# Optimization experiments

Hardware: AMD Instinct MI355X
Metric: run time of the kernel (lower is better)

Reference implementation:

```python
import jax, jax.numpy as jnp
import numpy as np

H = 1024      # hidden_size
E = 8         # num_experts
I = 1024      # moe_intermediate_size
SI = 2816     # shared_expert_intermediate_size
B, S = 2, 2048


def setup_inputs() -> dict:
    key = jax.random.key(0)
    ks = jax.random.split(key, 10)
    sc = lambda fan_in: 1.0 / np.sqrt(fan_in)
    return {
        "hidden_states": jax.random.normal(ks[0], (B, S, H), dtype=jnp.float32),
        "gate_w": jax.random.normal(ks[1], (E, H), dtype=jnp.float32) * sc(H),
        "wg": jax.random.normal(ks[2], (E, I, H), dtype=jnp.float32) * sc(H),   # gate_proj per expert
        "wu": jax.random.normal(ks[3], (E, I, H), dtype=jnp.float32) * sc(H),   # up_proj per expert
        "wd": jax.random.normal(ks[4], (E, H, I), dtype=jnp.float32) * sc(I),   # down_proj per expert
        "swg": jax.random.normal(ks[5], (SI, H), dtype=jnp.float32) * sc(H),    # shared gate_proj
        "swu": jax.random.normal(ks[6], (SI, H), dtype=jnp.float32) * sc(H),    # shared up_proj
        "swd": jax.random.normal(ks[7], (H, SI), dtype=jnp.float32) * sc(SI),   # shared down_proj
        "shared_gate_w": jax.random.normal(ks[8], (1, H), dtype=jnp.float32) * sc(H),
        "top_k": 2,
    }


def reference(hidden_states, gate_w, wg, wu, wd, swg, swu, swd, shared_gate_w, top_k):
    b, s, h = hidden_states.shape
    flat = hidden_states.reshape(-1, h)                      # [T,H]
    # router
    logits = flat @ gate_w.T                                 # [T,E]
    probs = jax.nn.softmax(logits, axis=-1)
    vals, idx = jax.lax.top_k(probs, top_k)                  # [T,K]
    vals = vals / jnp.sum(vals, axis=-1, keepdims=True)      # norm_topk_prob
    # combine weights scattered to full expert dim: [T,E]
    combine = jnp.sum(jax.nn.one_hot(idx, E, dtype=flat.dtype) * vals[..., None], axis=1)
    # dense per-expert SwiGLU FFN over all tokens, masked-combined (same math)
    g = jax.nn.silu(jnp.einsum("th,eih->eti", flat, wg))     # [E,T,I]
    u = jnp.einsum("th,eih->eti", flat, wu)
    eo = jnp.einsum("eti,ehi->eth", g * u, wd)               # [E,T,H]
    expert_out = jnp.einsum("te,eth->th", combine, eo)       # [T,H]
    # shared expert with sigmoid gate
    shared = (jax.nn.silu(flat @ swg.T) * (flat @ swu.T)) @ swd.T   # [T,H]
    sgate = jax.nn.sigmoid(flat @ shared_gate_w.T)           # [T,1]
    out = expert_out + sgate * shared
    return out.reshape(b, s, h)
```

## Files before the change

kernel.cpp:

```cpp
#include <hip/hip_runtime.h>
#include <stdint.h>

#define TT  4096
#define HD  1024
#define NE  8
#define ID  1024
#define SID 2816

typedef short s16x8 __attribute__((ext_vector_type(8)));
typedef float f32x4 __attribute__((ext_vector_type(4)));
typedef float f32x4v __attribute__((ext_vector_type(4)));
typedef unsigned short u16x4 __attribute__((ext_vector_type(4)));

__device__ __forceinline__ ushort f2bf(float f) {
  uint32_t u = __float_as_uint(f);
  u += 0x7FFFu + ((u >> 16) & 1u);
  return (ushort)(u >> 16);
}

__device__ __forceinline__ float bf2f(ushort u) {
  return __uint_as_float((uint32_t)u << 16);
}

__device__ __forceinline__ void gll16(const ushort* g, ushort* l) {
  __builtin_amdgcn_global_load_lds(
      (const __attribute__((address_space(1))) void*)g,
      (__attribute__((address_space(3))) void*)l, 16, 0, 0);
}

struct CvtArgs {
  const float* src[7];
  ushort* dst[7];
  int n[7];
};

__global__ __launch_bounds__(256) void cvt_all(CvtArgs a) {
  int t = blockIdx.y;
  int i = (blockIdx.x * 256 + threadIdx.x) * 4;
  if (i >= a.n[t]) return;
  f32x4v v = *(const f32x4v*)(a.src[t] + i);
  u16x4 o;
  o.x = f2bf(v.x); o.y = f2bf(v.y); o.z = f2bf(v.z); o.w = f2bf(v.w);
  *(u16x4*)(a.dst[t] + i) = o;
}

__global__ __launch_bounds__(256) void router_k(
    const float* __restrict__ X, const float* __restrict__ gw,
    const float* __restrict__ sgw,
    int* __restrict__ topki, float* __restrict__ topkw,
    float* __restrict__ sgate) {
  __shared__ float gwL[(NE + 1) * HD];
  #pragma unroll
  for (int i = 0; i < NE * HD / 1024; i++) {
    int idx = i * 1024 + threadIdx.x * 4;
    *(f32x4*)&gwL[idx] = *(const f32x4*)&gw[idx];
  }
  {
    int idx = threadIdx.x * 4;
    if (idx < HD) *(f32x4*)&gwL[NE * HD + idx] = *(const f32x4*)&sgw[idx];
  }
  __syncthreads();

  const int wave = threadIdx.x >> 6, lane = threadIdx.x & 63;
  #pragma unroll
  for (int tt = 0; tt < 4; tt++) {
    const int t = blockIdx.x * 16 + wave * 4 + tt;
    const float* x = X + (size_t)t * HD;
    float acc[NE + 1];
    #pragma unroll
    for (int e = 0; e <= NE; e++) acc[e] = 0.f;
    #pragma unroll
    for (int p = 0; p < HD / 256; p++) {
      const int k = p * 256 + lane * 4;
      f32x4 xv = *(const f32x4*)&x[k];
      #pragma unroll
      for (int e = 0; e < NE; e++) {
        f32x4 g = *(const f32x4*)&gwL[e * HD + k];
        acc[e] += xv.x * g.x + xv.y * g.y + xv.z * g.z + xv.w * g.w;
      }
      f32x4 s = *(const f32x4*)&gwL[NE * HD + k];
      acc[NE] += xv.x * s.x + xv.y * s.y + xv.z * s.z + xv.w * s.w;
    }
    #pragma unroll
    for (int off = 32; off > 0; off >>= 1)
      #pragma unroll
      for (int e = 0; e <= NE; e++)
        acc[e] += __shfl_xor(acc[e], off, 64);
    if (lane == 0) {
      float m = acc[0];
      #pragma unroll
      for (int e = 1; e < NE; e++) m = fmaxf(m, acc[e]);
      float p[NE];
      #pragma unroll
      for (int e = 0; e < NE; e++) p[e] = __expf(acc[e] - m);
      int i1 = 0;
      #pragma unroll
      for (int e = 1; e < NE; e++) if (p[e] > p[i1]) i1 = e;
      int i2 = (i1 == 0) ? 1 : 0;
      #pragma unroll
      for (int e = 0; e < NE; e++) if (e != i1 && p[e] > p[i2]) i2 = e;
      float inv = 1.f / (p[i1] + p[i2]);
      topki[2 * t] = i1; topki[2 * t + 1] = i2;
      topkw[2 * t] = p[i1] * inv; topkw[2 * t + 1] = p[i2] * inv;
      sgate[t] = 1.f / (1.f + __expf(-acc[NE]));
    }
  }
}

__global__ __launch_bounds__(1024) void binning_k(
    const int* __restrict__ topki, const float* __restrict__ topkw,
    int* __restrict__ cnt, int* __restrict__ offs,
    int* __restrict__ tokmap, float* __restrict__ wmap,
    int* __restrict__ smap) {
  __shared__ int h[NE];
  __shared__ int base[NE];
  const int tid = threadIdx.x;
  if (tid < NE) h[tid] = 0;
  __syncthreads();
  int my_e[8];
  #pragma unroll
  for (int i = 0; i < 8; i++) {
    int s = i * 1024 + tid;
    my_e[i] = topki[s];
    atomicAdd(&h[my_e[i]], 1);
  }
  __syncthreads();
  if (tid == 0) {
    int o = 0;
    for (int e = 0; e < NE; e++) {
      base[e] = o; offs[e] = o; cnt[e] = h[e]; o += h[e];
    }
  }
  __syncthreads();
  #pragma unroll
  for (int i = 0; i < 8; i++) {
    int s = i * 1024 + tid;
    int pos = atomicAdd(&base[my_e[i]], 1);
    tokmap[pos] = s >> 1;
    wmap[pos] = topkw[s];
    smap[s] = pos;
  }
}

constexpr int BM = 128, BN = 128, BK = 32;

template <bool GATHER>
__device__ __forceinline__ void gu_core(
    const ushort* __restrict__ A, const ushort* __restrict__ Wg,
    const ushort* __restrict__ Wu, ushort* __restrict__ Hout,
    const int* __restrict__ tokmap, int cnt, int seg,
    int mb, int nb, int N, int K) {
  const int m0 = mb * BM;
  if (m0 >= cnt) return;
  const int n0 = nb * BN;

  __shared__ ushort lA[3][BM * BK];
  __shared__ ushort lBg[3][BN * BK];
  __shared__ ushort lBu[3][BN * BK];

  const int tid = threadIdx.x;
  const int wave = tid >> 6, lane = tid & 63;
  const int wm = (wave >> 1) * 64, wn = (wave & 1) * 64;

  const int ar0 = wave * 32 + (lane >> 2);
  const int ar1 = ar0 + 16;
  const int kc = ((lane & 3) ^ ((lane >> 3) & 3)) * 8;

  const ushort *a0p, *a1p;
  if (GATHER) {
    int m_ = m0 + ar0;
    int tk0 = (m_ < cnt) ? tokmap[seg + m_] : 0;
    m_ = m0 + ar1;
    int tk1 = (m_ < cnt) ? tokmap[seg + m_] : 0;
    a0p = A + (size_t)tk0 * K + kc;
    a1p = A + (size_t)tk1 * K + kc;
  } else {
    a0p = A + (size_t)(m0 + ar0) * K + kc;
    a1p = A + (size_t)(m0 + ar1) * K + kc;
  }
  const ushort* bg0 = Wg + (size_t)(n0 + ar0) * K + kc;
  const ushort* bg1 = Wg + (size_t)(n0 + ar1) * K + kc;
  const ushort* bu0 = Wu + (size_t)(n0 + ar0) * K + kc;
  const ushort* bu1 = Wu + (size_t)(n0 + ar1) * K + kc;

  f32x4 accG[4][4], accU[4][4];
  #pragma unroll
  for (int i = 0; i < 4; i++)
    #pragma unroll
    for (int j = 0; j < 4; j++) {
      accG[i][j] = f32x4{0.f, 0.f, 0.f, 0.f};
      accU[i][j] = f32x4{0.f, 0.f, 0.f, 0.f};
    }

  const int lr = lane & 15;
  const int lk = (((lane >> 4) ^ ((lr >> 1) & 3))) * 8;
  const int w32 = wave * 32;

  auto stage = [&](int b, int k0) {
    gll16(a0p + k0, &lA[b][w32 * BK]);
    gll16(a1p + k0, &lA[b][(w32 + 16) * BK]);
    gll16(bg0 + k0, &lBg[b][w32 * BK]);
    gll16(bg1 + k0, &lBg[b][(w32 + 16) * BK]);
    gll16(bu0 + k0, &lBu[b][w32 * BK]);
    gll16(bu1 + k0, &lBu[b][(w32 + 16) * BK]);
  };

  const int nt = K / BK;
  stage(0, 0);
  stage(1, BK);
  int buf = 0;
  for (int t = 0; t < nt; t++) {
    if (t + 2 < nt) {
      int nb2 = buf + 2; if (nb2 >= 3) nb2 -= 3;
      stage(nb2, (t + 2) * BK);
      asm volatile("s_waitcnt vmcnt(12)" ::: "memory");
    } else if (t + 1 < nt) {
      asm volatile("s_waitcnt vmcnt(6)" ::: "memory");
    } else {
      asm volatile("s_waitcnt vmcnt(0)" ::: "memory");
    }
    __builtin_amdgcn_s_barrier();

    s16x8 af[4], bgf[4], buf_[4];
    #pragma unroll
    for (int i = 0; i < 4; i++) {
      af[i]   = *(const s16x8*)&lA [buf][(wm + i * 16 + lr) * BK + lk];
      bgf[i]  = *(const s16x8*)&lBg[buf][(wn + i * 16 + lr) * BK + lk];
      buf_[i] = *(const s16x8*)&lBu[buf][(wn + i * 16 + lr) * BK + lk];
    }
    #pragma unroll
    for (int i = 0; i < 4; i++)
      #pragma unroll
      for (int j = 0; j < 4; j++) {
        accG[i][j] = __builtin_amdgcn_mfma_f32_16x16x32_bf16(af[i], bgf[j], accG[i][j], 0, 0, 0);
        accU[i][j] = __builtin_amdgcn_mfma_f32_16x16x32_bf16(af[i], buf_[j], accU[i][j], 0, 0, 0);
      }
    __builtin_amdgcn_s_barrier();
    buf++; if (buf >= 3) buf = 0;
  }

  const int lrr = (lane >> 4) * 4;
  #pragma unroll
  for (int i = 0; i < 4; i++) {
    #pragma unroll
    for (int r = 0; r < 4; r++) {
      int m = wm + i * 16 + lrr + r;
      if (m0 + m < cnt) {
        size_t row = (size_t)(seg + m0 + m) * N;
        #pragma unroll
        for (int j = 0; j < 4; j++) {
          int c = n0 + wn + j * 16 + lr;
          float g = accG[i][j][r];
          float u = accU[i][j][r];
          float s = g / (1.f + __expf(-g));
          Hout[row + c] = f2bf(s * u);
        }
      }
    }
  }
}

template <bool GATHER>
__device__ __forceinline__ void dn_core(
    const ushort* __restrict__ A, const ushort* __restrict__ W,
    ushort* __restrict__ outB, float* __restrict__ outF,
    const float* __restrict__ sgate, int cnt, int seg,
    int mb, int nb, int N, int K) {
  const int m0 = mb * BM;
  if (m0 >= cnt) return;
  const int n0 = nb * BN;

  __shared__ ushort lA[3][BM * BK];
  __shared__ ushort lB[3][BN * BK];

  const int tid = threadIdx.x;
  const int wave = tid >> 6, lane = tid & 63;
  const int wm = (wave >> 1) * 64, wn = (wave & 1) * 64;

  const int ar0 = wave * 32 + (lane >> 2);
  const int ar1 = ar0 + 16;
  const int kc = ((lane & 3) ^ ((lane >> 3) & 3)) * 8;

  int r0 = m0 + ar0; if (r0 > cnt - 1) r0 = cnt - 1;
  int r1 = m0 + ar1; if (r1 > cnt - 1) r1 = cnt - 1;
  const ushort* a0p = A + (size_t)(seg + r0) * K + kc;
  const ushort* a1p = A + (size_t)(seg + r1) * K + kc;
  const ushort* b0 = W + (size_t)(n0 + ar0) * K + kc;
  const ushort* b1 = W + (size_t)(n0 + ar1) * K + kc;

  f32x4 acc[4][4];
  #pragma unroll
  for (int i = 0; i < 4; i++)
    #pragma unroll
    for (int j = 0; j < 4; j++) acc[i][j] = f32x4{0.f, 0.f, 0.f, 0.f};

  const int lr = lane & 15;
  const int lk = (((lane >> 4) ^ ((lr >> 1) & 3))) * 8;
  const int w32 = wave * 32;

  auto stage = [&](int b, int k0) {
    gll16(a0p + k0, &lA[b][w32 * BK]);
    gll16(a1p + k0, &lA[b][(w32 + 16) * BK]);
    gll16(b0 + k0, &lB[b][w32 * BK]);
    gll16(b1 + k0, &lB[b][(w32 + 16) * BK]);
  };

  const int nt = K / BK;
  stage(0, 0);
  stage(1, BK);
  int buf = 0;
  for (int t = 0; t < nt; t++) {
    if (t + 2 < nt) {
      int nb2 = buf + 2; if (nb2 >= 3) nb2 -= 3;
      stage(nb2, (t + 2) * BK);
      asm volatile("s_waitcnt vmcnt(8)" ::: "memory");
    } else if (t + 1 < nt) {
      asm volatile("s_waitcnt vmcnt(4)" ::: "memory");
    } else {
      asm volatile("s_waitcnt vmcnt(0)" ::: "memory");
    }
    __builtin_amdgcn_s_barrier();

    s16x8 af[4], bf[4];
    #pragma unroll
    for (int i = 0; i < 4; i++) {
      af[i] = *(const s16x8*)&lA[buf][(wm + i * 16 + lr) * BK + lk];
      bf[i] = *(const s16x8*)&lB[buf][(wn + i * 16 + lr) * BK + lk];
    }
    #pragma unroll
    for (int i = 0; i < 4; i++)
      #pragma unroll
      for (int j = 0; j < 4; j++)
        acc[i][j] = __builtin_amdgcn_mfma_f32_16x16x32_bf16(af[i], bf[j], acc[i][j], 0, 0, 0);
    __builtin_amdgcn_s_barrier();
    buf++; if (buf >= 3) buf = 0;
  }

  const int lrr = (lane >> 4) * 4;
  #pragma unroll
  for (int i = 0; i < 4; i++) {
    #pragma unroll
    for (int r = 0; r < 4; r++) {
      int m = wm + i * 16 + lrr + r;
      if (m0 + m < cnt) {
        if (GATHER) {
          size_t row = (size_t)(seg + m0 + m) * N;
          #pragma unroll
          for (int j = 0; j < 4; j++) {
            int c = n0 + wn + j * 16 + lr;
            outB[row + c] = f2bf(acc[i][j][r]);
          }
        } else {
          int t = m0 + m;
          float wv = sgate[t];
          size_t row = (size_t)t * N;
          #pragma unroll
          for (int j = 0; j < 4; j++) {
            int c = n0 + wn + j * 16 + lr;
            outF[row + c] = wv * acc[i][j][r];
          }
        }
      }
    }
  }
}

__global__ __launch_bounds__(256, 2) void gemm_gu_s(
    const ushort* __restrict__ A, const ushort* __restrict__ Wg,
    const ushort* __restrict__ Wu, ushort* __restrict__ H,
    int M, int N, int K, int nbn) {
  int nwg = gridDim.x, id = blockIdx.x;
  int lg = (id & 7) * (nwg >> 3) + (id >> 3);
  gu_core<false>(A, Wg, Wu, H, nullptr, M, 0, lg / nbn, lg % nbn, N, K);
}

__global__ __launch_bounds__(256, 2) void gemm_gu_r(
    const ushort* __restrict__ A, const ushort* __restrict__ Wg,
    const ushort* __restrict__ Wu, ushort* __restrict__ H,
    const int* __restrict__ tokmap, const int* __restrict__ cnts,
    const int* __restrict__ offs, int N, int K) {
  int e = blockIdx.x;
  gu_core<true>(A, Wg + (size_t)e * N * K, Wu + (size_t)e * N * K, H,
                tokmap, cnts[e], offs[e], blockIdx.y, blockIdx.z, N, K);
}

__global__ __launch_bounds__(256, 2) void gemm_dn_s(
    const ushort* __restrict__ A, const ushort* __restrict__ W,
    float* __restrict__ out, const float* __restrict__ sgate,
    int M, int N, int K, int nbn) {
  int nwg = gridDim.x, id = blockIdx.x;
  int lg = (id & 7) * (nwg >> 3) + (id >> 3);
  dn_core<false>(A, W, nullptr, out, sgate, M, 0, lg / nbn, lg % nbn, N, K);
}

__global__ __launch_bounds__(256, 2) void gemm_dn_r(
    const ushort* __restrict__ A, const ushort* __restrict__ W,
    ushort* __restrict__ eo, const int* __restrict__ cnts,
    const int* __restrict__ offs, int N, int K) {
  int e = blockIdx.x;
  dn_core<true>(A, W + (size_t)e * N * K, eo, nullptr, nullptr,
                cnts[e], offs[e], blockIdx.y, blockIdx.z, N, K);
}

__global__ __launch_bounds__(256) void combine_k(
    const ushort* __restrict__ eo, const float* __restrict__ topkw,
    const int* __restrict__ smap, float* __restrict__ out) {
  int t = blockIdx.x;
  int c = threadIdx.x * 4;
  int s0 = smap[2 * t], s1 = smap[2 * t + 1];
  float w0 = topkw[2 * t], w1 = topkw[2 * t + 1];
  u16x4 a = *(const u16x4*)&eo[(size_t)s0 * HD + c];
  u16x4 b = *(const u16x4*)&eo[(size_t)s1 * HD + c];
  float* o = out + (size_t)t * HD + c;
  f32x4 ov = *(const f32x4*)o;
  #pragma unroll
  for (int j = 0; j < 4; j++)
    ov[j] += w0 * bf2f(a[j]) + w1 * bf2f(b[j]);
  *(f32x4*)o = ov;
}

extern "C" void kernel_launch(void* const* d_in, const int* in_sizes, int n_in,
                              void* d_out, int out_size, void* d_ws, size_t ws_size,
                              hipStream_t stream) {
  const float* hs  = (const float*)d_in[0];
  const float* gw  = (const float*)d_in[1];
  const float* wg  = (const float*)d_in[2];
  const float* wu  = (const float*)d_in[3];
  const float* wd  = (const float*)d_in[4];
  const float* swg = (const float*)d_in[5];
  const float* swu = (const float*)d_in[6];
  const float* swd = (const float*)d_in[7];
  const float* sgw = (const float*)d_in[8];
  float* out = (float*)d_out;

  uint8_t* base = (uint8_t*)d_ws;
  size_t off = 0;
  auto give = [&](size_t b) -> void* {
    void* p = base + off;
    off += (b + 255) & ~(size_t)255;
    return p;
  };
  ushort* Xb   = (ushort*)give((size_t)TT * HD * 2);
  ushort* wgB  = (ushort*)give((size_t)NE * ID * HD * 2);
  ushort* wuB  = (ushort*)give((size_t)NE * ID * HD * 2);
  ushort* wdB  = (ushort*)give((size_t)NE * HD * ID * 2);
  ushort* sgB  = (ushort*)give((size_t)SID * HD * 2);
  ushort* suB  = (ushort*)give((size_t)SID * HD * 2);
  ushort* sdB  = (ushort*)give((size_t)HD * SID * 2);
  ushort* Sbuf = (ushort*)give((size_t)TT * SID * 2);
  ushort* Hbuf = (ushort*)give((size_t)2 * TT * ID * 2);
  float* sgate = (float*)give(TT * 4);
  int* topki   = (int*)give(TT * 2 * 4);
  float* topkw = (float*)give(TT * 2 * 4);
  int* tokmap  = (int*)give(2 * TT * 4);
  float* wmap  = (float*)give(2 * TT * 4);
  int* smap    = (int*)give(2 * TT * 4);
  int* cnt     = (int*)give(256);
  int* offs    = (int*)give(256);

  CvtArgs ca;
  ca.src[0] = hs;  ca.dst[0] = Xb;  ca.n[0] = TT * HD;
  ca.src[1] = wg;  ca.dst[1] = wgB; ca.n[1] = NE * ID * HD;
  ca.src[2] = wu;  ca.dst[2] = wuB; ca.n[2] = NE * ID * HD;
  ca.src[3] = wd;  ca.dst[3] = wdB; ca.n[3] = NE * HD * ID;
  ca.src[4] = swg; ca.dst[4] = sgB; ca.n[4] = SID * HD;
  ca.src[5] = swu; ca.dst[5] = suB; ca.n[5] = SID * HD;
  ca.src[6] = swd; ca.dst[6] = sdB; ca.n[6] = HD * SID;
  cvt_all<<<dim3(8192, 7), 256, 0, stream>>>(ca);

  router_k<<<TT / 16, 256, 0, stream>>>(hs, gw, sgw, topki, topkw, sgate);
  binning_k<<<1, 1024, 0, stream>>>(topki, topkw, cnt, offs, tokmap, wmap, smap);

  gemm_gu_s<<<(TT / BM) * (SID / BN), 256, 0, stream>>>(
      Xb, sgB, suB, Sbuf, TT, SID, HD, SID / BN);
  gemm_dn_s<<<(TT / BM) * (HD / BN), 256, 0, stream>>>(
      Sbuf, sdB, out, sgate, TT, HD, SID, HD / BN);

  gemm_gu_r<<<dim3(NE, 2 * TT / BM, ID / BN), 256, 0, stream>>>(
      Xb, wgB, wuB, Hbuf, tokmap, cnt, offs, ID, HD);
  gemm_dn_r<<<dim3(NE, 2 * TT / BM, HD / BN), 256, 0, stream>>>(
      Hbuf, wdB, Sbuf , cnt, offs, HD, ID);

  combine_k<<<TT, 256, 0, stream>>>(Sbuf, topkw, smap, out);
}
```

Baseline: 286.7 us.

## Switch GEMM cores to double buffering and retile shared-expert block mapping

Reduces the LDS pipeline in both GEMM cores from triple to double buffering, prefetching one K-tile ahead instead of two. This cuts LDS usage, which could raise occupancy, at the cost of less latency hiding for global loads. The shared-expert kernels also replace the generic XCD-interleaved block index with a hard-coded mapping that groups M and N tiles per XCD for better L2 reuse. That mapping assumes the fixed grid sizes (32x22 and 32x8).

```diff
diff --git a/kernel.cpp b/kernel.cpp
--- a/kernel.cpp
+++ b/kernel.cpp
@@ -154,9 +154,9 @@
   if (m0 >= cnt) return;
   const int n0 = nb * BN;
 
-  __shared__ ushort lA[3][BM * BK];
-  __shared__ ushort lBg[3][BN * BK];
-  __shared__ ushort lBu[3][BN * BK];
+  __shared__ ushort lA[2][BM * BK];
+  __shared__ ushort lBg[2][BN * BK];
+  __shared__ ushort lBu[2][BN * BK];
 
   const int tid = threadIdx.x;
   const int wave = tid >> 6, lane = tid & 63;
@@ -207,14 +207,10 @@
 
   const int nt = K / BK;
   stage(0, 0);
-  stage(1, BK);
-  int buf = 0;
   for (int t = 0; t < nt; t++) {
-    if (t + 2 < nt) {
-      int nb2 = buf + 2; if (nb2 >= 3) nb2 -= 3;
-      stage(nb2, (t + 2) * BK);
-      asm volatile("s_waitcnt vmcnt(12)" ::: "memory");
-    } else if (t + 1 < nt) {
+    const int cur = t & 1;
+    if (t + 1 < nt) {
+      stage(cur ^ 1, (t + 1) * BK);
       asm volatile("s_waitcnt vmcnt(6)" ::: "memory");
     } else {
       asm volatile("s_waitcnt vmcnt(0)" ::: "memory");
@@ -224,9 +220,9 @@
     s16x8 af[4], bgf[4], buf_[4];
     #pragma unroll
     for (int i = 0; i < 4; i++) {
-      af[i]   = *(const s16x8*)&lA [buf][(wm + i * 16 + lr) * BK + lk];
-      bgf[i]  = *(const s16x8*)&lBg[buf][(wn + i * 16 + lr) * BK + lk];
-      buf_[i] = *(const s16x8*)&lBu[buf][(wn + i * 16 + lr) * BK + lk];
+      af[i]   = *(const s16x8*)&lA [cur][(wm + i * 16 + lr) * BK + lk];
+      bgf[i]  = *(const s16x8*)&lBg[cur][(wn + i * 16 + lr) * BK + lk];
+      buf_[i] = *(const s16x8*)&lBu[cur][(wn + i * 16 + lr) * BK + lk];
     }
     #pragma unroll
     for (int i = 0; i < 4; i++)
@@ -236,7 +232,6 @@
         accU[i][j] = __builtin_amdgcn_mfma_f32_16x16x32_bf16(af[i], buf_[j], accU[i][j], 0, 0, 0);
       }
     __builtin_amdgcn_s_barrier();
-    buf++; if (buf >= 3) buf = 0;
   }
 
   const int lrr = (lane >> 4) * 4;
@@ -270,8 +265,8 @@
   if (m0 >= cnt) return;
   const int n0 = nb * BN;
 
-  __shared__ ushort lA[3][BM * BK];
-  __shared__ ushort lB[3][BN * BK];
+  __shared__ ushort lA[2][BM * BK];
+  __shared__ ushort lB[2][BN * BK];
 
   const int tid = threadIdx.x;
   const int wave = tid >> 6, lane = tid & 63;
@@ -307,14 +302,10 @@
 
   const int nt = K / BK;
   stage(0, 0);
-  stage(1, BK);
-  int buf = 0;
   for (int t = 0; t < nt; t++) {
-    if (t + 2 < nt) {
-      int nb2 = buf + 2; if (nb2 >= 3) nb2 -= 3;
-      stage(nb2, (t + 2) * BK);
-      asm volatile("s_waitcnt vmcnt(8)" ::: "memory");
-    } else if (t + 1 < nt) {
+    const int cur = t & 1;
+    if (t + 1 < nt) {
+      stage(cur ^ 1, (t + 1) * BK);
       asm volatile("s_waitcnt vmcnt(4)" ::: "memory");
     } else {
       asm volatile("s_waitcnt vmcnt(0)" ::: "memory");
@@ -324,8 +315,8 @@
     s16x8 af[4], bf[4];
     #pragma unroll
     for (int i = 0; i < 4; i++) {
-      af[i] = *(const s16x8*)&lA[buf][(wm + i * 16 + lr) * BK + lk];
-      bf[i] = *(const s16x8*)&lB[buf][(wn + i * 16 + lr) * BK + lk];
+      af[i] = *(const s16x8*)&lA[cur][(wm + i * 16 + lr) * BK + lk];
+      bf[i] = *(const s16x8*)&lB[cur][(wn + i * 16 + lr) * BK + lk];
     }
     #pragma unroll
     for (int i = 0; i < 4; i++)
@@ -333,7 +324,6 @@
       for (int j = 0; j < 4; j++)
         acc[i][j] = __builtin_amdgcn_mfma_f32_16x16x32_bf16(af[i], bf[j], acc[i][j], 0, 0, 0);
     __builtin_amdgcn_s_barrier();
-    buf++; if (buf >= 3) buf = 0;
   }
 
   const int lrr = (lane >> 4) * 4;
@@ -368,10 +358,12 @@
 __global__ __launch_bounds__(256, 2) void gemm_gu_s(
     const ushort* __restrict__ A, const ushort* __restrict__ Wg,
     const ushort* __restrict__ Wu, ushort* __restrict__ H,
-    int M, int N, int K, int nbn) {
-  int nwg = gridDim.x, id = blockIdx.x;
-  int lg = (id & 7) * (nwg >> 3) + (id >> 3);
-  gu_core<false>(A, Wg, Wu, H, nullptr, M, 0, lg / nbn, lg % nbn, N, K);
+    int M, int N, int K) {
+  int id = blockIdx.x;
+  int x = id & 7, k = id >> 3;
+  int mb = (x & 3) * 8 + (k & 7);
+  int nb = (x >> 2) * 11 + (k >> 3);
+  gu_core<false>(A, Wg, Wu, H, nullptr, M, 0, mb, nb, N, K);
 }
 
 __global__ __launch_bounds__(256, 2) void gemm_gu_r(
@@ -387,10 +379,12 @@
 __global__ __launch_bounds__(256, 2) void gemm_dn_s(
     const ushort* __restrict__ A, const ushort* __restrict__ W,
     float* __restrict__ out, const float* __restrict__ sgate,
-    int M, int N, int K, int nbn) {
-  int nwg = gridDim.x, id = blockIdx.x;
-  int lg = (id & 7) * (nwg >> 3) + (id >> 3);
-  dn_core<false>(A, W, nullptr, out, sgate, M, 0, lg / nbn, lg % nbn, N, K);
+    int M, int N, int K) {
+  int id = blockIdx.x;
+  int x = id & 7, k = id >> 3;
+  int mb = x * 4 + (k & 3);
+  int nb = k >> 2;
+  dn_core<false>(A, W, nullptr, out, sgate, M, 0, mb, nb, N, K);
 }
 
 __global__ __launch_bounds__(256, 2) void gemm_dn_r(
@@ -472,9 +466,9 @@
   binning_k<<<1, 1024, 0, stream>>>(topki, topkw, cnt, offs, tokmap, wmap, smap);
 
   gemm_gu_s<<<(TT / BM) * (SID / BN), 256, 0, stream>>>(
-      Xb, sgB, suB, Sbuf, TT, SID, HD, SID / BN);
+      Xb, sgB, suB, Sbuf, TT, SID, HD);
   gemm_dn_s<<<(TT / BM) * (HD / BN), 256, 0, stream>>>(
-      Sbuf, sdB, out, sgate, TT, HD, SID, HD / BN);
+      Sbuf, sdB, out, sgate, TT, HD, SID);
 
   gemm_gu_r<<<dim3(NE, 2 * TT / BM, ID / BN), 256, 0, stream>>>(
       Xb, wgB, wuB, Hbuf, tokmap, cnt, offs, ID, HD);
```

Result: no change. 288.5 us (+0.6%).
